# Kernel tuning notes

Measured on AMD Instinct MI355X. Metric: run time of the kernel, lower is better.

The kernel has to match this reference:

```python
import jax, jax.numpy as jnp
import numpy as np

EPS = 1e-12  # torch F.normalize default eps


def setup_inputs() -> dict:
    key = jax.random.key(0)
    k1, k2, k3, k4 = jax.random.split(key, 4)
    N, F_IN, F_OUT = 8192, 128, 128
    x = jax.random.normal(k1, (N, F_IN), dtype=jnp.float32)
    adj = jax.random.uniform(k2, (N, N), dtype=jnp.float32)
    # fc_layer params (xavier_uniform with relu gain for W, default-ish bias)
    gain = float(np.sqrt(2.0))
    limit = gain * float(np.sqrt(6.0 / (F_IN + F_OUT)))
    W = jax.random.uniform(k3, (F_OUT, F_IN), dtype=jnp.float32, minval=-limit, maxval=limit)
    b = jax.random.uniform(k4, (F_OUT,), dtype=jnp.float32, minval=-1.0 / np.sqrt(F_IN), maxval=1.0 / np.sqrt(F_IN))
    return {"x": x, "adj": adj, "W": W, "b": b}


def reference(x, adj, W, b):
    N = adj.shape[0]
    # A' = A + I (self loops)
    a = adj + jnp.eye(N, dtype=adj.dtype)
    # degree normalization D^-1/2 A' D^-1/2 as a fused broadcast scale
    # (the torch code does this via two dense diag matmuls; same math)
    dinv = jax.lax.rsqrt(jnp.sum(a, axis=-1))  # [N]
    a = a * dinv[:, None] * dinv[None, :]
    # aggregation + linear
    h = a @ x                    # [N, F_IN]
    h = h @ W.T + b              # [N, F_OUT]
    # F.normalize(dim=1): L2 normalize each row
    norm = jnp.linalg.norm(h, axis=1, keepdims=True)
    return h / jnp.maximum(norm, EPS)
```

## Files before the change

### kernel.cpp

```cpp
#include <hip/hip_runtime.h>
#include <hip/hip_bf16.h>


typedef __attribute__((ext_vector_type(8))) short short8;
typedef __attribute__((ext_vector_type(4))) float f32x4;
typedef __attribute__((ext_vector_type(4))) unsigned short us4;

static __device__ __forceinline__ unsigned short f2bf(float f) {
    unsigned int u = __float_as_uint(f);
    u += 0x7FFFu + ((u >> 16) & 1u);
    return (unsigned short)(u >> 16);
}

__global__ __launch_bounds__(512) void gcn_prep(
    const float* __restrict__ adj, const float* __restrict__ x,
    const float* __restrict__ W,
    unsigned short* __restrict__ yT, float* __restrict__ dinv,
    unsigned short* __restrict__ Wb)
{
    const int tid = threadIdx.x;
    const int blk = blockIdx.x;
    if (blk >= 256) {
        int idx = (blk - 256) * 512 + tid;
        Wb[idx] = f2bf(W[idx]);
        return;
    }
    const int wave = tid >> 6;
    const int lane = tid & 63;
    const long j0 = (long)blk * 32;

    __shared__ float s_di[32];

    for (int r = 0; r < 4; ++r) {
        const long j = j0 + wave * 4 + r;
        const float4* row = (const float4*)(adj + j * 8192L);
        float s = 0.f;
#pragma unroll
        for (int it = 0; it < 32; ++it) {
            float4 v = row[it * 64 + lane];
            s += (v.x + v.y) + (v.z + v.w);
        }
        for (int off = 1; off < 64; off <<= 1) s += __shfl_xor(s, off, 64);
        if (lane == 0) s_di[wave * 4 + r] = rsqrtf(s + 1.0f);
    }
    __syncthreads();
    if (tid < 32) dinv[j0 + tid] = s_di[tid];

    const int jj = tid & 31;
    const int fb = tid >> 5;
    const float di = s_di[jj];
#pragma unroll
    for (int p = 0; p < 8; ++p) {
        int f = p * 16 + fb;
        yT[(long)f * 8192 + j0 + jj] = f2bf(di * x[(j0 + jj) * 128 + f]);
    }
}

#define M_TILE 32
#define BKC    512
#define NCHUNK 16

__global__ __launch_bounds__(512, 1) void gcn_main(
    const float* __restrict__ adj, const float* __restrict__ x,
    const float* __restrict__ bias,
    const unsigned short* __restrict__ yT, const float* __restrict__ dinv,
    const unsigned short* __restrict__ Wb, float* __restrict__ out)
{
    __shared__ unsigned short Ab[2][M_TILE][BKC];

    const int tid  = threadIdx.x;
    const int wave = tid >> 6;
    const int lane = tid & 63;
    const int q    = lane >> 4;
    const int ln   = lane & 15;
    const int nb   = wave * 16;
    const long rowBase = (long)blockIdx.x * M_TILE;

    f32x4 acc[2] = {};
    float4 st[8];

    auto load_chunk = [&](int c) {
#pragma unroll
        for (int i = 0; i < 8; ++i) {
            int t   = wave * 8 + i;
            int row = t >> 1;
            int col = ((t & 1) << 8) + (lane << 2);
            st[i] = *(const float4*)&adj[(rowBase + row) * 8192L + (long)c * BKC + col];
        }
    };
    auto write_chunk = [&](int buf) {
#pragma unroll
        for (int i = 0; i < 8; ++i) {
            int t   = wave * 8 + i;
            int row = t >> 1;
            int col = ((t & 1) << 8) + (lane << 2);
            us4 w4;
            w4.x = f2bf(st[i].x); w4.y = f2bf(st[i].y);
            w4.z = f2bf(st[i].z); w4.w = f2bf(st[i].w);
            *(us4*)&Ab[buf][row][col] = w4;
        }
    };

    load_chunk(0);
    write_chunk(0);
    __syncthreads();

#pragma unroll 1
    for (int c = 0; c < NCHUNK; ++c) {
        const int cur = c & 1;
        if (c + 1 < NCHUNK) load_chunk(c + 1);
#pragma unroll 4
        for (int s = 0; s < BKC / 32; ++s) {
            const int k0 = s * 32 + q * 8;
            short8 a0 = *(const short8*)&Ab[cur][ln][k0];
            short8 a1 = *(const short8*)&Ab[cur][16 + ln][k0];
            const long kg = (long)c * BKC + k0;
            short8 b0 = *(const short8*)&yT[(nb + ln) * 8192L + kg];
            acc[0] = __builtin_amdgcn_mfma_f32_16x16x32_bf16(a0, b0, acc[0], 0, 0, 0);
            acc[1] = __builtin_amdgcn_mfma_f32_16x16x32_bf16(a1, b0, acc[1], 0, 0, 0);
        }
        if (c + 1 < NCHUNK) write_chunk(cur ^ 1);
        __syncthreads();
    }

    unsigned short* t_lds = &Ab[0][0][0];
    float* s_dinv = (float*)(t_lds + 32 * 136);
    float* s_part = s_dinv + 32;
    float* s_inv  = s_part + 256;

    if (tid < 32) s_dinv[tid] = dinv[rowBase + tid];
    __syncthreads();

#pragma unroll
    for (int mi = 0; mi < 2; ++mi)
#pragma unroll
        for (int r = 0; r < 4; ++r) {
            int m = mi * 16 + q * 4 + r;
            int n = nb + ln;
            float di = s_dinv[m];
            float tv = di * acc[mi][r] + di * di * x[(rowBase + m) * 128 + n];
            t_lds[m * 136 + n] = f2bf(tv);
        }
    __syncthreads();

    f32x4 z[2] = {};
#pragma unroll
    for (int s = 0; s < 4; ++s) {
        const int k0 = s * 32 + q * 8;
        short8 a0 = *(const short8*)&t_lds[ln * 136 + k0];
        short8 a1 = *(const short8*)&t_lds[(16 + ln) * 136 + k0];
        short8 b0 = *(const short8*)&Wb[(nb + ln) * 128 + k0];
        z[0] = __builtin_amdgcn_mfma_f32_16x16x32_bf16(a0, b0, z[0], 0, 0, 0);
        z[1] = __builtin_amdgcn_mfma_f32_16x16x32_bf16(a1, b0, z[1], 0, 0, 0);
    }

    float bv0 = bias[nb + ln];
    float zv[2][4];
    float rp[2][4];
#pragma unroll
    for (int mi = 0; mi < 2; ++mi)
#pragma unroll
        for (int r = 0; r < 4; ++r) {
            float v0 = z[mi][r] + bv0;
            zv[mi][r] = v0;
            rp[mi][r] = v0 * v0;
        }
#pragma unroll
    for (int mi = 0; mi < 2; ++mi)
#pragma unroll
        for (int r = 0; r < 4; ++r)
            for (int off = 1; off < 16; off <<= 1)
                rp[mi][r] += __shfl_xor(rp[mi][r], off, 64);
    if (ln == 0) {
#pragma unroll
        for (int mi = 0; mi < 2; ++mi)
#pragma unroll
            for (int r = 0; r < 4; ++r)
                s_part[(mi * 16 + q * 4 + r) * 8 + wave] = rp[mi][r];
    }
    __syncthreads();
    if (tid < 32) {
        float s = 0.f;
#pragma unroll
        for (int w = 0; w < 8; ++w) s += s_part[tid * 8 + w];
        float nrm = sqrtf(s);
        s_inv[tid] = 1.0f / fmaxf(nrm, 1e-12f);
    }
    __syncthreads();

#pragma unroll
    for (int mi = 0; mi < 2; ++mi)
#pragma unroll
        for (int r = 0; r < 4; ++r) {
            int m = mi * 16 + q * 4 + r;
            int n = nb + ln;
            out[(rowBase + m) * 128 + n] = zv[mi][r] * s_inv[m];
        }
}

extern "C" void kernel_launch(void* const* d_in, const int* in_sizes, int n_in,
                              void* d_out, int out_size, void* d_ws, size_t ws_size,
                              hipStream_t stream) {
    const float* x   = (const float*)d_in[0];
    const float* adj = (const float*)d_in[1];
    const float* W   = (const float*)d_in[2];
    const float* b   = (const float*)d_in[3];
    float* out = (float*)d_out;

    unsigned short* yT  = (unsigned short*)d_ws;
    float*          dv  = (float*)((char*)d_ws + (2u << 20));
    unsigned short* Wb  = (unsigned short*)((char*)d_ws + (2u << 20) + 32768);

    gcn_prep<<<256 + 32, 512, 0, stream>>>(adj, x, W, yT, dv, Wb);
    gcn_main<<<256, 512, 0, stream>>>(adj, x, b, yT, dv, Wb, out);
}
```

Before: 471.5 us.

## Halve row tile to 16, double grid, swizzle LDS to avoid bank conflicts

The main kernel's row tile shrinks from 32 to 16 rows and the K-chunk from 512 to 256. The grid doubles to 512 blocks, so all 256 CUs get two blocks and occupancy can rise (launch bounds now allow 4 blocks per CU). The LDS adjacency tile gets an XOR swizzle to reduce bank conflicts on the MFMA A-operand reads. The cost is that each block now reuses the yT B-operand across only one 16-row MFMA tile, which doubles global/L2 traffic for yT, and there are twice as many chunk barriers.

```diff
diff --git a/kernel.cpp b/kernel.cpp
--- a/kernel.cpp
+++ b/kernel.cpp
@@ -56,17 +56,19 @@
     }
 }
 
-#define M_TILE 32
-#define BKC    512
-#define NCHUNK 16
+#define M_TILE 16
+#define BKC    256
+#define NCHUNK 32
 
-__global__ __launch_bounds__(512, 1) void gcn_main(
+#define SWZ(r, c) ((r) * BKC + ((c) ^ (((r) & 7) << 3)))
+
+__global__ __launch_bounds__(512, 4) void gcn_main(
     const float* __restrict__ adj, const float* __restrict__ x,
     const float* __restrict__ bias,
     const unsigned short* __restrict__ yT, const float* __restrict__ dinv,
     const unsigned short* __restrict__ Wb, float* __restrict__ out)
 {
-    __shared__ unsigned short Ab[2][M_TILE][BKC];
+    __shared__ unsigned short Ab[2][M_TILE * BKC];
 
     const int tid  = threadIdx.x;
     const int wave = tid >> 6;
@@ -76,28 +78,24 @@
     const int nb   = wave * 16;
     const long rowBase = (long)blockIdx.x * M_TILE;
 
-    f32x4 acc[2] = {};
-    float4 st[8];
+    f32x4 acc = {};
+    float4 st[2];
 
     auto load_chunk = [&](int c) {
 #pragma unroll
-        for (int i = 0; i < 8; ++i) {
-            int t   = wave * 8 + i;
-            int row = t >> 1;
-            int col = ((t & 1) << 8) + (lane << 2);
-            st[i] = *(const float4*)&adj[(rowBase + row) * 8192L + (long)c * BKC + col];
+        for (int i = 0; i < 2; ++i) {
+            int row = wave + i * 8;
+            st[i] = *(const float4*)&adj[(rowBase + row) * 8192L + (long)c * BKC + lane * 4];
         }
     };
     auto write_chunk = [&](int buf) {
 #pragma unroll
-        for (int i = 0; i < 8; ++i) {
-            int t   = wave * 8 + i;
-            int row = t >> 1;
-            int col = ((t & 1) << 8) + (lane << 2);
+        for (int i = 0; i < 2; ++i) {
+            int row = wave + i * 8;
             us4 w4;
             w4.x = f2bf(st[i].x); w4.y = f2bf(st[i].y);
             w4.z = f2bf(st[i].z); w4.w = f2bf(st[i].w);
-            *(us4*)&Ab[buf][row][col] = w4;
+            *(us4*)&Ab[buf][SWZ(row, lane * 4)] = w4;
         }
     };
 
@@ -109,77 +107,63 @@
     for (int c = 0; c < NCHUNK; ++c) {
         const int cur = c & 1;
         if (c + 1 < NCHUNK) load_chunk(c + 1);
-#pragma unroll 4
+#pragma unroll
         for (int s = 0; s < BKC / 32; ++s) {
             const int k0 = s * 32 + q * 8;
-            short8 a0 = *(const short8*)&Ab[cur][ln][k0];
-            short8 a1 = *(const short8*)&Ab[cur][16 + ln][k0];
-            const long kg = (long)c * BKC + k0;
-            short8 b0 = *(const short8*)&yT[(nb + ln) * 8192L + kg];
-            acc[0] = __builtin_amdgcn_mfma_f32_16x16x32_bf16(a0, b0, acc[0], 0, 0, 0);
-            acc[1] = __builtin_amdgcn_mfma_f32_16x16x32_bf16(a1, b0, acc[1], 0, 0, 0);
+            short8 a = *(const short8*)&Ab[cur][SWZ(ln, k0)];
+            short8 b = *(const short8*)&yT[(nb + ln) * 8192L + (long)c * BKC + k0];
+            acc = __builtin_amdgcn_mfma_f32_16x16x32_bf16(a, b, acc, 0, 0, 0);
         }
         if (c + 1 < NCHUNK) write_chunk(cur ^ 1);
         __syncthreads();
     }
 
-    unsigned short* t_lds = &Ab[0][0][0];
-    float* s_dinv = (float*)(t_lds + 32 * 136);
-    float* s_part = s_dinv + 32;
-    float* s_inv  = s_part + 256;
+    unsigned short* t_lds = &Ab[0][0];
+    float* s_dinv = (float*)(t_lds + 16 * 136);
+    float* s_part = s_dinv + 16;
+    float* s_inv  = s_part + 128;
 
-    if (tid < 32) s_dinv[tid] = dinv[rowBase + tid];
+    if (tid < 16) s_dinv[tid] = dinv[rowBase + tid];
     __syncthreads();
 
 #pragma unroll
-    for (int mi = 0; mi < 2; ++mi)
-#pragma unroll
-        for (int r = 0; r < 4; ++r) {
-            int m = mi * 16 + q * 4 + r;
-            int n = nb + ln;
-            float di = s_dinv[m];
-            float tv = di * acc[mi][r] + di * di * x[(rowBase + m) * 128 + n];
-            t_lds[m * 136 + n] = f2bf(tv);
-        }
+    for (int r = 0; r < 4; ++r) {
+        int m = q * 4 + r;
+        int n = nb + ln;
+        float di = s_dinv[m];
+        float tv = di * acc[r] + di * di * x[(rowBase + m) * 128 + n];
+        t_lds[m * 136 + n] = f2bf(tv);
+    }
     __syncthreads();
 
-    f32x4 z[2] = {};
+    f32x4 z = {};
 #pragma unroll
     for (int s = 0; s < 4; ++s) {
         const int k0 = s * 32 + q * 8;
-        short8 a0 = *(const short8*)&t_lds[ln * 136 + k0];
-        short8 a1 = *(const short8*)&t_lds[(16 + ln) * 136 + k0];
-        short8 b0 = *(const short8*)&Wb[(nb + ln) * 128 + k0];
-        z[0] = __builtin_amdgcn_mfma_f32_16x16x32_bf16(a0, b0, z[0], 0, 0, 0);
-        z[1] = __builtin_amdgcn_mfma_f32_16x16x32_bf16(a1, b0, z[1], 0, 0, 0);
+        short8 a = *(const short8*)&t_lds[ln * 136 + k0];
+        short8 b = *(const short8*)&Wb[(nb + ln) * 128 + k0];
+        z = __builtin_amdgcn_mfma_f32_16x16x32_bf16(a, b, z, 0, 0, 0);
     }
 
-    float bv0 = bias[nb + ln];
-    float zv[2][4];
-    float rp[2][4];
+    float bv = bias[nb + ln];
+    float zv[4], rp[4];
 #pragma unroll
-    for (int mi = 0; mi < 2; ++mi)
+    for (int r = 0; r < 4; ++r) {
+        float v = z[r] + bv;
+        zv[r] = v;
+        rp[r] = v * v;
+    }
 #pragma unroll
-        for (int r = 0; r < 4; ++r) {
-            float v0 = z[mi][r] + bv0;
-            zv[mi][r] = v0;
-            rp[mi][r] = v0 * v0;
-        }
-#pragma unroll
-    for (int mi = 0; mi < 2; ++mi)
+    for (int r = 0; r < 4; ++r)
+        for (int off = 1; off < 16; off <<= 1)
+            rp[r] += __shfl_xor(rp[r], off, 64);
+    if (ln == 0) {
 #pragma unroll
         for (int r = 0; r < 4; ++r)
-            for (int off = 1; off < 16; off <<= 1)
-                rp[mi][r] += __shfl_xor(rp[mi][r], off, 64);
-    if (ln == 0) {
-#pragma unroll
-        for (int mi = 0; mi < 2; ++mi)
-#pragma unroll
-            for (int r = 0; r < 4; ++r)
-                s_part[(mi * 16 + q * 4 + r) * 8 + wave] = rp[mi][r];
+            s_part[(q * 4 + r) * 8 + wave] = rp[r];
     }
     __syncthreads();
-    if (tid < 32) {
+    if (tid < 16) {
         float s = 0.f;
 #pragma unroll
         for (int w = 0; w < 8; ++w) s += s_part[tid * 8 + w];
@@ -189,13 +173,10 @@
     __syncthreads();
 
 #pragma unroll
-    for (int mi = 0; mi < 2; ++mi)
-#pragma unroll
-        for (int r = 0; r < 4; ++r) {
-            int m = mi * 16 + q * 4 + r;
-            int n = nb + ln;
-            out[(rowBase + m) * 128 + n] = zv[mi][r] * s_inv[m];
-        }
+    for (int r = 0; r < 4; ++r) {
+        int m = q * 4 + r;
+        out[(rowBase + m) * 128 + nb + ln] = zv[r] * s_inv[m];
+    }
 }
 
 extern "C" void kernel_launch(void* const* d_in, const int* in_sizes, int n_in,
@@ -212,5 +193,5 @@
     unsigned short* Wb  = (unsigned short*)((char*)d_ws + (2u << 20) + 32768);
 
     gcn_prep<<<256 + 32, 512, 0, stream>>>(adj, x, W, yT, dv, Wb);
-    gcn_main<<<256, 512, 0, stream>>>(adj, x, b, yT, dv, Wb, out);
+    gcn_main<<<512, 512, 0, stream>>>(adj, x, b, yT, dv, Wb, out);
 }
```

Measured after the change: 508.7 us. 7.9% more time.

## Pre-convert adjacency to MFMA-tiled bf16 in prep, stream via global_load_lds

Applied to the files above, without the earlier changes.

The prep kernel now converts each adjacency row to bf16 while it computes the row sum, and writes it in a layout tiled to match the MFMA A-operand. The main kernel streams these bf16 tiles straight into LDS with global_load_lds, replacing fp32 loads plus in-register conversion. Main-kernel adjacency traffic halves, but prep must write a 128 MB bf16 copy that main then reads back. Whether the extra write and read beat two fp32 reads depends on cache residency.

```diff
diff --git a/kernel.cpp b/kernel.cpp
--- a/kernel.cpp
+++ b/kernel.cpp
@@ -12,11 +12,17 @@
     return (unsigned short)(u >> 16);
 }
 
+static __device__ __forceinline__ void gload16(const void* g, const void* l) {
+    __builtin_amdgcn_global_load_lds(
+        (const __attribute__((address_space(1))) unsigned int*)g,
+        (__attribute__((address_space(3))) unsigned int*)l, 16, 0, 0);
+}
+
 __global__ __launch_bounds__(512) void gcn_prep(
     const float* __restrict__ adj, const float* __restrict__ x,
     const float* __restrict__ W,
     unsigned short* __restrict__ yT, float* __restrict__ dinv,
-    unsigned short* __restrict__ Wb)
+    unsigned short* __restrict__ Wb, unsigned short* __restrict__ adjb)
 {
     const int tid = threadIdx.x;
     const int blk = blockIdx.x;
@@ -25,105 +31,101 @@
         Wb[idx] = f2bf(W[idx]);
         return;
     }
-    const int wave = tid >> 6;
-    const int lane = tid & 63;
+    const int wave   = tid >> 6;
+    const int lane   = tid & 63;
+    const int rowsel = lane >> 4;
+    const int l16    = lane & 15;
     const long j0 = (long)blk * 32;
+    const long j  = j0 + wave * 4 + rowsel;
+    const int rt = (int)(j >> 4);
+    const int ln = (int)(j & 15);
+    const int q  = (l16 >> 1) & 3;
+    const int jj = (l16 & 1) * 4;
 
     __shared__ float s_di[32];
 
-    for (int r = 0; r < 4; ++r) {
-        const long j = j0 + wave * 4 + r;
-        const float4* row = (const float4*)(adj + j * 8192L);
-        float s = 0.f;
-#pragma unroll
-        for (int it = 0; it < 32; ++it) {
-            float4 v = row[it * 64 + lane];
-            s += (v.x + v.y) + (v.z + v.w);
-        }
-        for (int off = 1; off < 64; off <<= 1) s += __shfl_xor(s, off, 64);
-        if (lane == 0) s_di[wave * 4 + r] = rsqrtf(s + 1.0f);
-    }
+    const float4* rowp = (const float4*)(adj + j * 8192L);
+    float s = 0.f;
+#pragma unroll 8
+    for (int it = 0; it < 128; ++it) {
+        float4 v = rowp[it * 16 + l16];
+        s += (v.x + v.y) + (v.z + v.w);
+        int ks = it * 2 + (l16 >> 3);
+        us4 w4;
+        w4.x = f2bf(v.x); w4.y = f2bf(v.y);
+        w4.z = f2bf(v.z); w4.w = f2bf(v.w);
+        *(us4*)&adjb[(((long)rt * 256 + ks) * 64 + q * 16 + ln) * 8 + jj] = w4;
+    }
+    s += __shfl_xor(s, 1, 64);
+    s += __shfl_xor(s, 2, 64);
+    s += __shfl_xor(s, 4, 64);
+    s += __shfl_xor(s, 8, 64);
+    if (l16 == 0) s_di[wave * 4 + rowsel] = rsqrtf(s + 1.0f);
     __syncthreads();
     if (tid < 32) dinv[j0 + tid] = s_di[tid];
 
-    const int jj = tid & 31;
+    const int jy = tid & 31;
     const int fb = tid >> 5;
-    const float di = s_di[jj];
+    const float di = s_di[jy];
 #pragma unroll
     for (int p = 0; p < 8; ++p) {
         int f = p * 16 + fb;
-        yT[(long)f * 8192 + j0 + jj] = f2bf(di * x[(j0 + jj) * 128 + f]);
-    }
-}
-
-#define M_TILE 32
-#define BKC    512
+        yT[(long)f * 8192 + j0 + jy] = f2bf(di * x[(j0 + jy) * 128 + f]);
+    }
+}
+
+#define CK 16
 #define NCHUNK 16
 
-__global__ __launch_bounds__(512, 1) void gcn_main(
-    const float* __restrict__ adj, const float* __restrict__ x,
+__global__ __launch_bounds__(512) void gcn_main(
+    const unsigned short* __restrict__ adjb, const float* __restrict__ x,
     const float* __restrict__ bias,
     const unsigned short* __restrict__ yT, const float* __restrict__ dinv,
     const unsigned short* __restrict__ Wb, float* __restrict__ out)
 {
-    __shared__ unsigned short Ab[2][M_TILE][BKC];
+    __shared__ unsigned short AbS[2][32 * 512];
 
     const int tid  = threadIdx.x;
     const int wave = tid >> 6;
     const int lane = tid & 63;
     const int q    = lane >> 4;
     const int ln   = lane & 15;
-    const int nb   = wave * 16;
-    const long rowBase = (long)blockIdx.x * M_TILE;
+    const int blk  = blockIdx.x;
+    const long rowBase = (long)blk * 32;
 
     f32x4 acc[2] = {};
-    float4 st[8];
-
-    auto load_chunk = [&](int c) {
-#pragma unroll
-        for (int i = 0; i < 8; ++i) {
-            int t   = wave * 8 + i;
-            int row = t >> 1;
-            int col = ((t & 1) << 8) + (lane << 2);
-            st[i] = *(const float4*)&adj[(rowBase + row) * 8192L + (long)c * BKC + col];
+
+    auto stage = [&](int c, int buf) {
+#pragma unroll
+        for (int i = 0; i < 4; ++i) {
+            int s = i * 8 + wave;
+            const char* src = (const char*)adjb +
+                ((((long)(blk * 2 + (s >> 4))) * 256 + c * CK + (s & 15)) * 64 + lane) * 16;
+            gload16(src, &AbS[buf][s * 512]);
         }
     };
-    auto write_chunk = [&](int buf) {
-#pragma unroll
-        for (int i = 0; i < 8; ++i) {
-            int t   = wave * 8 + i;
-            int row = t >> 1;
-            int col = ((t & 1) << 8) + (lane << 2);
-            us4 w4;
-            w4.x = f2bf(st[i].x); w4.y = f2bf(st[i].y);
-            w4.z = f2bf(st[i].z); w4.w = f2bf(st[i].w);
-            *(us4*)&Ab[buf][row][col] = w4;
-        }
-    };
-
-    load_chunk(0);
-    write_chunk(0);
-    __syncthreads();
+
+    stage(0, 0);
+    __syncthreads();
+
+    const unsigned short* bcol = &yT[(wave * 16 + ln) * 8192L + q * 8];
 
 #pragma unroll 1
     for (int c = 0; c < NCHUNK; ++c) {
         const int cur = c & 1;
-        if (c + 1 < NCHUNK) load_chunk(c + 1);
-#pragma unroll 4
-        for (int s = 0; s < BKC / 32; ++s) {
-            const int k0 = s * 32 + q * 8;
-            short8 a0 = *(const short8*)&Ab[cur][ln][k0];
-            short8 a1 = *(const short8*)&Ab[cur][16 + ln][k0];
-            const long kg = (long)c * BKC + k0;
-            short8 b0 = *(const short8*)&yT[(nb + ln) * 8192L + kg];
-            acc[0] = __builtin_amdgcn_mfma_f32_16x16x32_bf16(a0, b0, acc[0], 0, 0, 0);
-            acc[1] = __builtin_amdgcn_mfma_f32_16x16x32_bf16(a1, b0, acc[1], 0, 0, 0);
-        }
-        if (c + 1 < NCHUNK) write_chunk(cur ^ 1);
+        if (c + 1 < NCHUNK) stage(c + 1, cur ^ 1);
+#pragma unroll
+        for (int ks = 0; ks < CK; ++ks) {
+            short8 a0 = *(const short8*)&AbS[cur][ks * 512 + lane * 8];
+            short8 a1 = *(const short8*)&AbS[cur][(16 + ks) * 512 + lane * 8];
+            short8 b  = *(const short8*)&bcol[c * 512 + ks * 32];
+            acc[0] = __builtin_amdgcn_mfma_f32_16x16x32_bf16(a0, b, acc[0], 0, 0, 0);
+            acc[1] = __builtin_amdgcn_mfma_f32_16x16x32_bf16(a1, b, acc[1], 0, 0, 0);
+        }
         __syncthreads();
     }
 
-    unsigned short* t_lds = &Ab[0][0][0];
+    unsigned short* t_lds = &AbS[0][0];
     float* s_dinv = (float*)(t_lds + 32 * 136);
     float* s_part = s_dinv + 32;
     float* s_inv  = s_part + 256;
@@ -132,13 +134,13 @@
     __syncthreads();
 
 #pragma unroll
-    for (int mi = 0; mi < 2; ++mi)
-#pragma unroll
-        for (int r = 0; r < 4; ++r) {
-            int m = mi * 16 + q * 4 + r;
-            int n = nb + ln;
+    for (int rt = 0; rt < 2; ++rt)
+#pragma unroll
+        for (int r = 0; r < 4; ++r) {
+            int m = rt * 16 + q * 4 + r;
+            int n = wave * 16 + ln;
             float di = s_dinv[m];
-            float tv = di * acc[mi][r] + di * di * x[(rowBase + m) * 128 + n];
+            float tv = di * acc[rt][r] + di * di * x[(rowBase + m) * 128 + n];
             t_lds[m * 136 + n] = f2bf(tv);
         }
     __syncthreads();
@@ -149,52 +151,52 @@
         const int k0 = s * 32 + q * 8;
         short8 a0 = *(const short8*)&t_lds[ln * 136 + k0];
         short8 a1 = *(const short8*)&t_lds[(16 + ln) * 136 + k0];
-        short8 b0 = *(const short8*)&Wb[(nb + ln) * 128 + k0];
-        z[0] = __builtin_amdgcn_mfma_f32_16x16x32_bf16(a0, b0, z[0], 0, 0, 0);
-        z[1] = __builtin_amdgcn_mfma_f32_16x16x32_bf16(a1, b0, z[1], 0, 0, 0);
-    }
-
-    float bv0 = bias[nb + ln];
-    float zv[2][4];
-    float rp[2][4];
-#pragma unroll
-    for (int mi = 0; mi < 2; ++mi)
-#pragma unroll
-        for (int r = 0; r < 4; ++r) {
-            float v0 = z[mi][r] + bv0;
-            zv[mi][r] = v0;
-            rp[mi][r] = v0 * v0;
-        }
-#pragma unroll
-    for (int mi = 0; mi < 2; ++mi)
-#pragma unroll
-        for (int r = 0; r < 4; ++r)
-            for (int off = 1; off < 16; off <<= 1)
-                rp[mi][r] += __shfl_xor(rp[mi][r], off, 64);
+        short8 b  = *(const short8*)&Wb[(wave * 16 + ln) * 128 + k0];
+        z[0] = __builtin_amdgcn_mfma_f32_16x16x32_bf16(a0, b, z[0], 0, 0, 0);
+        z[1] = __builtin_amdgcn_mfma_f32_16x16x32_bf16(a1, b, z[1], 0, 0, 0);
+    }
+
+    float bv = bias[wave * 16 + ln];
+    float zv[2][4], rp[2][4];
+#pragma unroll
+    for (int rt = 0; rt < 2; ++rt)
+#pragma unroll
+        for (int r = 0; r < 4; ++r) {
+            float v = z[rt][r] + bv;
+            zv[rt][r] = v;
+            rp[rt][r] = v * v;
+        }
+#pragma unroll
+    for (int rt = 0; rt < 2; ++rt)
+#pragma unroll
+        for (int r = 0; r < 4; ++r) {
+            rp[rt][r] += __shfl_xor(rp[rt][r], 1, 64);
+            rp[rt][r] += __shfl_xor(rp[rt][r], 2, 64);
+            rp[rt][r] += __shfl_xor(rp[rt][r], 4, 64);
+            rp[rt][r] += __shfl_xor(rp[rt][r], 8, 64);
+        }
     if (ln == 0) {
 #pragma unroll
-        for (int mi = 0; mi < 2; ++mi)
+        for (int rt = 0; rt < 2; ++rt)
 #pragma unroll
             for (int r = 0; r < 4; ++r)
-                s_part[(mi * 16 + q * 4 + r) * 8 + wave] = rp[mi][r];
+                s_part[(rt * 16 + q * 4 + r) * 8 + wave] = rp[rt][r];
     }
     __syncthreads();
     if (tid < 32) {
         float s = 0.f;
 #pragma unroll
         for (int w = 0; w < 8; ++w) s += s_part[tid * 8 + w];
-        float nrm = sqrtf(s);
-        s_inv[tid] = 1.0f / fmaxf(nrm, 1e-12f);
-    }
-    __syncthreads();
-
-#pragma unroll
-    for (int mi = 0; mi < 2; ++mi)
-#pragma unroll
-        for (int r = 0; r < 4; ++r) {
-            int m = mi * 16 + q * 4 + r;
-            int n = nb + ln;
-            out[(rowBase + m) * 128 + n] = zv[mi][r] * s_inv[m];
+        s_inv[tid] = 1.0f / fmaxf(sqrtf(s), 1e-12f);
+    }
+    __syncthreads();
+
+#pragma unroll
+    for (int rt = 0; rt < 2; ++rt)
+#pragma unroll
+        for (int r = 0; r < 4; ++r) {
+            int m = rt * 16 + q * 4 + r;
+            out[(rowBase + m) * 128 + wave * 16 + ln] = zv[rt][r] * s_inv[m];
         }
 }
 
@@ -207,10 +209,11 @@
     const float* b   = (const float*)d_in[3];
     float* out = (float*)d_out;
 
-    unsigned short* yT  = (unsigned short*)d_ws;
-    float*          dv  = (float*)((char*)d_ws + (2u << 20));
-    unsigned short* Wb  = (unsigned short*)((char*)d_ws + (2u << 20) + 32768);
-
-    gcn_prep<<<256 + 32, 512, 0, stream>>>(adj, x, W, yT, dv, Wb);
-    gcn_main<<<256, 512, 0, stream>>>(adj, x, b, yT, dv, Wb, out);
-}
+    unsigned short* yT   = (unsigned short*)d_ws;
+    float*          dv   = (float*)((char*)d_ws + (2u << 20));
+    unsigned short* Wb   = (unsigned short*)((char*)d_ws + (2u << 20) + 32768);
+    unsigned short* adjb = (unsigned short*)((char*)d_ws + (4u << 20));
+
+    gcn_prep<<<256 + 32, 512, 0, stream>>>(adj, x, W, yT, dv, Wb, adjb);
+    gcn_main<<<256, 512, 0, stream>>>(adjb, x, b, yT, dv, Wb, out);
+}
```

Result: faster. 459.4 us (-2.6%).
